# Optimization experiments

Measured on AMD Instinct MI355X. Metric: run time of the kernel, lower is better.

## Reference

```python
import jax, jax.numpy as jnp
import numpy as np

SEQ, D, H, FF = 2048, 1024, 16, 4096
HD = D // H  # head_dim = 64


def setup_inputs() -> dict:
    key = jax.random.key(0)
    ks = jax.random.split(key, 13)
    s = lambda k, shape, fan_in: jax.random.normal(k, shape, jnp.float32) / np.sqrt(fan_in)
    return {
        "x":  jax.random.normal(ks[0], (SEQ, D), jnp.float32),
        # per-head Q/K/V linears, batched over the head axis: [H, D, HD]
        "Wq": s(ks[1], (H, D, HD), D), "bq": jnp.zeros((H, HD), jnp.float32),
        "Wk": s(ks[2], (H, D, HD), D), "bk": jnp.zeros((H, HD), jnp.float32),
        "Wv": s(ks[3], (H, D, HD), D), "bv": jnp.zeros((H, HD), jnp.float32),
        "Wp": s(ks[4], (D, D), D),     "bp": jnp.zeros((D,), jnp.float32),
        "W1": s(ks[5], (D, FF), D),    "b1": jnp.zeros((FF,), jnp.float32),
        "W2": s(ks[6], (FF, D), FF),   "b2": jnp.zeros((D,), jnp.float32),
    }


def reference(x, Wq, bq, Wk, bk, Wv, bv, Wp, bp, W1, b1, W2, b2):
    # Batched per-head projections: [H, S, HD]
    Qx = jnp.einsum("sd,hde->hse", x, Wq) + bq[:, None, :]
    Kx = jnp.einsum("sd,hde->hse", x, Wk) + bk[:, None, :]
    Vx = jnp.einsum("sd,hde->hse", x, Wv) + bv[:, None, :]
    # scores[h,s,t] = Qx[h,s]. Kx[h,t] / sqrt(HD); softmax over t (last dim)
    scores = jnp.einsum("hse,hte->hst", Qx, Kx) / jnp.sqrt(jnp.float32(HD))
    attn = jax.nn.softmax(scores, axis=-1)
    # Faithful to source: head[t,e] = sum_s Vx[s,e] * attn[s,t]  (attn^T @ V)
    heads = jnp.einsum("hse,hst->hte", Vx, attn)  # [H, S, HD]
    # concat heads along feature dim (head-major order) -> [S, D]
    concat = jnp.transpose(heads, (1, 0, 2)).reshape(SEQ, H * HD)
    proj = concat @ Wp + bp
    hidden = jax.nn.relu(proj @ W1 + b1)
    out = hidden @ W2 + b2
    return out
```

## Files before the change

kernel.cpp:

```cpp
#include <hip/hip_runtime.h>
#include <math.h>

constexpr int S_  = 2048;
constexpr int D_  = 1024;
constexpr int H_  = 16;
constexpr int HD_ = 64;
constexpr int FF_ = 4096;

typedef short bf16x8 __attribute__((ext_vector_type(8)));
typedef float f32x4  __attribute__((ext_vector_type(4)));

static __device__ __forceinline__ ushort f2bf(float f) {
    union { __bf16 b; ushort u; } c;
    c.b = (__bf16)f;
    return c.u;
}
static __device__ __forceinline__ float bf2f(ushort u) {
    return __uint_as_float(((unsigned)u) << 16);
}

static __device__ __forceinline__ float exp8(float x) {
    return __builtin_amdgcn_exp2f(x * 0.18033688f);
}

static __device__ __forceinline__ void gload_lds16(const void* g, void* l) {
    __builtin_amdgcn_global_load_lds(
        (const __attribute__((address_space(1))) unsigned int*)g,
        (__attribute__((address_space(3))) unsigned int*)l, 16, 0, 0);
}

static __device__ __forceinline__ void tc_tile(
    const float* __restrict__ in, ushort* __restrict__ out,
    int K, int N, int n0, int k0)
{
    __shared__ float Ts[32][33];
    const int tid = threadIdx.x;
    const int r = tid >> 3, c4 = (tid & 7) * 4;
    float4 v = *(const float4*)(in + (size_t)(k0 + r) * N + n0 + c4);
    Ts[r][c4 + 0] = v.x; Ts[r][c4 + 1] = v.y;
    Ts[r][c4 + 2] = v.z; Ts[r][c4 + 3] = v.w;
    __syncthreads();
    ushort4 o;
    o.x = f2bf(Ts[c4 + 0][r]); o.y = f2bf(Ts[c4 + 1][r]);
    o.z = f2bf(Ts[c4 + 2][r]); o.w = f2bf(Ts[c4 + 3][r]);
    *(ushort4*)(out + (size_t)(n0 + r) * K + k0 + c4) = o;
}

__global__ __launch_bounds__(256) void pack_all(
    const float* __restrict__ x,
    const float* __restrict__ Wq, const float* __restrict__ Wk,
    const float* __restrict__ Wv, const float* __restrict__ Wp,
    const float* __restrict__ W1, const float* __restrict__ W2,
    const float* __restrict__ bq, const float* __restrict__ bk,
    const float* __restrict__ bv,
    ushort* __restrict__ xb, ushort* __restrict__ BTqkv,
    ushort* __restrict__ BTp, ushort* __restrict__ BT1,
    ushort* __restrict__ BT2, float* __restrict__ biascat)
{
    const int b = blockIdx.x;
    const int tid = threadIdx.x;
    if (b < 2048) {
        const int i = b * 1024 + tid * 4;
        float4 v = *(const float4*)(x + i);
        ushort4 o;
        o.x = f2bf(v.x); o.y = f2bf(v.y); o.z = f2bf(v.z); o.w = f2bf(v.w);
        *(ushort4*)(xb + i) = o;
    } else if (b < 5120) {
        int j = b - 2048;
        const int which = j >> 10;
        j &= 1023;
        const int hh = j >> 6, t = j & 63;
        const float* W = (which == 0) ? Wq : (which == 1) ? Wk : Wv;
        tc_tile(W + hh * 65536, BTqkv + which * 1024 * 1024 + hh * 65536,
                1024, 64, (t & 1) * 32, (t >> 1) * 32);
    } else if (b < 6144) {
        const int j = b - 5120;
        tc_tile(Wp, BTp, 1024, 1024, (j & 31) * 32, (j >> 5) * 32);
    } else if (b < 10240) {
        const int j = b - 6144;
        tc_tile(W1, BT1, 1024, 4096, (j & 127) * 32, (j >> 7) * 32);
    } else if (b < 14336) {
        const int j = b - 10240;
        tc_tile(W2, BT2, 4096, 1024, (j & 31) * 32, (j >> 5) * 32);
    } else {
        const int i = (b - 14336) * 256 + tid;
        float v = (i < 1024) ? bq[i] : (i < 2048 ? bk[i - 1024] : bv[i - 2048]);
        biascat[i] = v;
    }
}

template <int BM, int BN, int WR, int WC, int KS, int RELU, int OUT>
__global__ __launch_bounds__(WR * WC * 64) void gemm_mfma(
    const ushort* __restrict__ A, const ushort* __restrict__ BT,
    const float* __restrict__ bias, void* __restrict__ Cv,
    void* __restrict__ Cv2, int M, int N, int K)
{
    constexpr int WAVES = WR * WC;
    constexpr int WTM = BM / WR, WTN = BN / WC;
    constexpr int MT = WTM / 16, NT = WTN / 16;
    constexpr int AI = BM / 8;
    constexpr int TI = (BM + BN) / 8;
    constexpr int PW = TI / WAVES;

    __shared__ ushort As[BM * 64];
    __shared__ ushort Bs[BN * 64];

    const int tid = threadIdx.x;
    const int lane = tid & 63;
    const int wave = tid >> 6;
    const int wr = wave / WC, wc = wave % WC;
    const int row16 = lane & 15, kgrp = lane >> 4;
    const int m0 = blockIdx.y * BM, n0 = blockIdx.x * BN;
    const int kOff = (KS > 1) ? blockIdx.z * (K / KS) : 0;

    const int lrow = lane >> 3;
    const int sc8 = (lane & 7) ^ lrow;

    f32x4 acc[MT][NT];
#pragma unroll
    for (int i = 0; i < MT; ++i)
#pragma unroll
        for (int j = 0; j < NT; ++j) acc[i][j] = (f32x4){0.f, 0.f, 0.f, 0.f};

    for (int k0 = kOff; k0 < kOff + K / KS; k0 += 64) {
        __syncthreads();
#pragma unroll
        for (int i = 0; i < PW; ++i) {
            const int inst = wave * PW + i;
            if (inst < AI) {
                const int row = inst * 8;
                gload_lds16(A + (size_t)(m0 + row + lrow) * K + k0 + sc8 * 8,
                            As + row * 64);
            } else {
                const int row = (inst - AI) * 8;
                gload_lds16(BT + (size_t)(n0 + row + lrow) * K + k0 + sc8 * 8,
                            Bs + row * 64);
            }
        }
        __syncthreads();
#pragma unroll
        for (int ks = 0; ks < 2; ++ks) {
            bf16x8 af[MT], bfr[NT];
#pragma unroll
            for (int mt = 0; mt < MT; ++mt) {
                const int r = wr * WTM + mt * 16 + row16;
                af[mt] = *(const bf16x8*)(As + r * 64 + (((ks * 4 + kgrp) ^ (r & 7)) * 8));
            }
#pragma unroll
            for (int nt = 0; nt < NT; ++nt) {
                const int r = wc * WTN + nt * 16 + row16;
                bfr[nt] = *(const bf16x8*)(Bs + r * 64 + (((ks * 4 + kgrp) ^ (r & 7)) * 8));
            }
#pragma unroll
            for (int mt = 0; mt < MT; ++mt)
#pragma unroll
                for (int nt = 0; nt < NT; ++nt)
                    acc[mt][nt] = __builtin_amdgcn_mfma_f32_16x16x32_bf16(
                        af[mt], bfr[nt], acc[mt][nt], 0, 0, 0);
        }
    }

    if constexpr (OUT == 2) {
        float* Cp = ((blockIdx.z < KS / 2) ? (float*)Cv : (float*)Cv2)
                    + (size_t)(blockIdx.z % (KS / 2)) * M * N;
#pragma unroll
        for (int nt = 0; nt < NT; ++nt) {
            const int n = n0 + wc * WTN + nt * 16 + row16;
#pragma unroll
            for (int mt = 0; mt < MT; ++mt)
#pragma unroll
                for (int r = 0; r < 4; ++r) {
                    const int m = m0 + wr * WTM + mt * 16 + kgrp * 4 + r;
                    Cp[(size_t)m * N + n] = acc[mt][nt][r];
                }
        }
    } else if constexpr (OUT == 3) {
        ushort* QKo = (ushort*)Cv;
        ushort* VTo = (ushort*)Cv2;
        if (n0 < 2048) {
#pragma unroll
            for (int nt = 0; nt < NT; ++nt) {
                const int n = n0 + wc * WTN + nt * 16 + row16;
                const float bb = bias[n];
#pragma unroll
                for (int mt = 0; mt < MT; ++mt)
#pragma unroll
                    for (int r = 0; r < 4; ++r) {
                        const int m = m0 + wr * WTM + mt * 16 + kgrp * 4 + r;
                        QKo[(size_t)m * 2048 + n] = f2bf(acc[mt][nt][r] + bb);
                    }
            }
        } else {
#pragma unroll
            for (int nt = 0; nt < NT; ++nt) {
                const int n = n0 + wc * WTN + nt * 16 + row16;
                const float bb = bias[n];
#pragma unroll
                for (int mt = 0; mt < MT; ++mt) {
                    const int mb = m0 + wr * WTM + mt * 16 + kgrp * 4;
                    ushort4 o;
                    o.x = f2bf(acc[mt][nt][0] + bb);
                    o.y = f2bf(acc[mt][nt][1] + bb);
                    o.z = f2bf(acc[mt][nt][2] + bb);
                    o.w = f2bf(acc[mt][nt][3] + bb);
                    *(ushort4*)(VTo + (size_t)(n - 2048) * 2048 + mb) = o;
                }
            }
        }
    } else {
#pragma unroll
        for (int nt = 0; nt < NT; ++nt) {
            const int n = n0 + wc * WTN + nt * 16 + row16;
            const float bb = bias ? bias[n] : 0.f;
#pragma unroll
            for (int mt = 0; mt < MT; ++mt)
#pragma unroll
                for (int r = 0; r < 4; ++r) {
                    const int m = m0 + wr * WTM + mt * 16 + kgrp * 4 + r;
                    float v = acc[mt][nt][r] + bb;
                    if (RELU) v = fmaxf(v, 0.f);
                    if (OUT == 1)
                        ((ushort*)Cv)[(size_t)m * N + n] = f2bf(v);
                    else
                        ((float*)Cv)[(size_t)m * N + n] = v;
                }
        }
    }
}

__global__ __launch_bounds__(256) void reduce4_bias(
    const float* __restrict__ pA, const float* __restrict__ pB,
    const float* __restrict__ bias, float* __restrict__ out, int MN, int N)
{
    const int i = (blockIdx.x * 256 + threadIdx.x) * 4;
    float4 a = *(const float4*)(pA + i);
    const float4 b = *(const float4*)(pA + (size_t)MN + i);
    const float4 c = *(const float4*)(pB + i);
    const float4 d = *(const float4*)(pB + (size_t)MN + i);
    const float4 e = *(const float4*)(bias + (i & (N - 1)));
    a.x += b.x + c.x + d.x + e.x;
    a.y += b.y + c.y + d.y + e.y;
    a.z += b.z + c.z + d.z + e.z;
    a.w += b.w + c.w + d.w + e.w;
    *(float4*)(out + i) = a;
}

__global__ __launch_bounds__(256) void reduce2_bias_bf16(
    const float* __restrict__ pA, const float* __restrict__ pB,
    const float* __restrict__ bias, ushort* __restrict__ out, int N)
{
    const int i = (blockIdx.x * 256 + threadIdx.x) * 4;
    const float4 a = *(const float4*)(pA + i);
    const float4 b = *(const float4*)(pB + i);
    const float4 e = *(const float4*)(bias + (i & (N - 1)));
    ushort4 o;
    o.x = f2bf(a.x + b.x + e.x);
    o.y = f2bf(a.y + b.y + e.y);
    o.z = f2bf(a.z + b.z + e.z);
    o.w = f2bf(a.w + b.w + e.w);
    *(ushort4*)(out + i) = o;
}

__global__ __launch_bounds__(256) void attn_stats(
    const ushort* __restrict__ QK, float* __restrict__ part)
{
    const int h = blockIdx.y;
    const int s0 = blockIdx.x * 128;
    const int tz = blockIdx.z;
    const int tid = threadIdx.x;
    const int lane = tid & 63;
    const int w = tid >> 6;
    const int row16 = lane & 15;
    const int kgrp = lane >> 4;

    __shared__ ushort Ks[64 * 64];

    bf16x8 qf[2][2];
#pragma unroll
    for (int mt = 0; mt < 2; ++mt) {
        const ushort* qp = QK + (size_t)(s0 + w * 32 + mt * 16 + row16) * 2048 + h * 64;
        qf[mt][0] = *(const bf16x8*)(qp + kgrp * 8);
        qf[mt][1] = *(const bf16x8*)(qp + kgrp * 8 + 32);
    }

    float suml[2][4] = {{0.f}};
    const int lr = lane >> 3;
    const int sw8 = ((lane & 7) ^ lr) * 8;

    for (int ti = 0; ti < 8; ++ti) {
        const int t0 = tz * 512 + ti * 64;
        __syncthreads();
#pragma unroll
        for (int i = 0; i < 2; ++i) {
            const int inst = w * 2 + i;
            gload_lds16(QK + (size_t)(t0 + inst * 8 + lr) * 2048 + 1024 + h * 64 + sw8,
                        Ks + inst * 512);
        }
        __syncthreads();
#pragma unroll
        for (int nt = 0; nt < 4; ++nt) {
            const int kr = nt * 16 + row16;
            bf16x8 kf0 = *(const bf16x8*)(Ks + kr * 64 + ((kgrp ^ (kr & 7)) * 8));
            bf16x8 kf1 = *(const bf16x8*)(Ks + kr * 64 + (((kgrp + 4) ^ (kr & 7)) * 8));
#pragma unroll
            for (int mt = 0; mt < 2; ++mt) {
                f32x4 sc = (f32x4){0.f, 0.f, 0.f, 0.f};
                sc = __builtin_amdgcn_mfma_f32_16x16x32_bf16(qf[mt][0], kf0, sc, 0, 0, 0);
                sc = __builtin_amdgcn_mfma_f32_16x16x32_bf16(qf[mt][1], kf1, sc, 0, 0, 0);
#pragma unroll
                for (int r = 0; r < 4; ++r)
                    suml[mt][r] += exp8(sc[r]);
            }
        }
    }
#pragma unroll
    for (int mt = 0; mt < 2; ++mt)
#pragma unroll
        for (int r = 0; r < 4; ++r) {
#pragma unroll
            for (int m = 1; m < 16; m <<= 1)
                suml[mt][r] += __shfl_xor(suml[mt][r], m, 64);
        }
    if (row16 == 0) {
#pragma unroll
        for (int mt = 0; mt < 2; ++mt)
#pragma unroll
            for (int r = 0; r < 4; ++r)
                part[((size_t)tz * H_ + h) * S_ + s0 + w * 32 + mt * 16 + kgrp * 4 + r]
                    = suml[mt][r];
    }
}

__global__ __launch_bounds__(256) void vscale_fused(
    ushort* __restrict__ VT, const float* __restrict__ statsP)
{
    const int s0 = blockIdx.x * 128;
    const int h = blockIdx.y;
    const int tid = threadIdx.x;
    __shared__ float il[128];
    if (tid < 128) {
        const int HS = H_ * S_;
        const int idx = h * S_ + s0 + tid;
        float s = statsP[idx] + statsP[HS + idx] +
                  statsP[2 * HS + idx] + statsP[3 * HS + idx];
        il[tid] = 1.f / s;
    }
    __syncthreads();
#pragma unroll
    for (int c = tid; c < 1024; c += 256) {
        const int row = c >> 4, cc = (c & 15) * 8;
        const size_t off = (size_t)(h * 64 + row) * 2048 + s0 + cc;
        union { uint4 u; ushort s[8]; } v;
        v.u = *(const uint4*)(VT + off);
#pragma unroll
        for (int j = 0; j < 8; ++j)
            v.s[j] = f2bf(bf2f(v.s[j]) * il[cc + j]);
        *(uint4*)(VT + off) = v.u;
    }
}

__global__ __launch_bounds__(256) void attn_pv(
    const ushort* __restrict__ QK, const ushort* __restrict__ VT,
    ushort* __restrict__ pvp)
{
    const int h = blockIdx.y;
    const int t0 = blockIdx.x * 128;
    const int sbase = blockIdx.z * 512;
    const int tid = threadIdx.x;
    const int lane = tid & 63;
    const int w = tid >> 6;
    const int row16 = lane & 15;
    const int kgrp = lane >> 4;

    __shared__ ushort KP[128 * 64];
    __shared__ ushort Qs[64 * 64];
    __shared__ ushort Vs[64 * 64];

    const int lr = lane >> 3;
    const int sw8 = ((lane & 7) ^ lr) * 8;

#pragma unroll
    for (int i = 0; i < 4; ++i) {
        const int inst = w * 4 + i;
        gload_lds16(QK + (size_t)(t0 + inst * 8 + lr) * 2048 + 1024 + h * 64 + sw8,
                    KP + inst * 512);
    }
    __syncthreads();
    bf16x8 kf[8][2];
#pragma unroll
    for (int nt = 0; nt < 8; ++nt) {
        const int r = nt * 16 + row16;
        kf[nt][0] = *(const bf16x8*)(KP + r * 64 + ((kgrp ^ (r & 7)) * 8));
        kf[nt][1] = *(const bf16x8*)(KP + r * 64 + (((kgrp + 4) ^ (r & 7)) * 8));
    }

    f32x4 acc[2][4];
#pragma unroll
    for (int i = 0; i < 2; ++i)
#pragma unroll
        for (int j = 0; j < 4; ++j) acc[i][j] = (f32x4){0.f, 0.f, 0.f, 0.f};

    for (int si = 0; si < 8; ++si) {
        const int s0 = sbase + si * 64;
        __syncthreads();
#pragma unroll
        for (int i = 0; i < 2; ++i) {
            const int inst = w * 2 + i;
            const int r = inst * 8 + lr;
            gload_lds16(QK + (size_t)(s0 + r) * 2048 + h * 64 + sw8,
                        Qs + inst * 512);
            gload_lds16(VT + (size_t)(h * 64 + r) * 2048 + s0 + sw8,
                        Vs + inst * 512);
        }
        __syncthreads();

        const int qr = w * 16 + row16;
        bf16x8 qf0 = *(const bf16x8*)(Qs + qr * 64 + ((kgrp ^ (qr & 7)) * 8));
        bf16x8 qf1 = *(const bf16x8*)(Qs + qr * 64 + (((kgrp + 4) ^ (qr & 7)) * 8));
#pragma unroll
        for (int nt = 0; nt < 8; ++nt) {
            f32x4 sc = (f32x4){0.f, 0.f, 0.f, 0.f};
            sc = __builtin_amdgcn_mfma_f32_16x16x32_bf16(qf0, kf[nt][0], sc, 0, 0, 0);
            sc = __builtin_amdgcn_mfma_f32_16x16x32_bf16(qf1, kf[nt][1], sc, 0, 0, 0);
            ushort4 o;
            o.x = f2bf(exp8(sc[0]));
            o.y = f2bf(exp8(sc[1]));
            o.z = f2bf(exp8(sc[2]));
            o.w = f2bf(exp8(sc[3]));
            const int tl = nt * 16 + row16;
            const int chunk = w * 2 + (kgrp >> 1);
            *(ushort4*)(KP + tl * 64 + ((chunk ^ (tl & 7)) * 8) + (kgrp & 1) * 4) = o;
        }
        __syncthreads();

        bf16x8 vf[4][2];
#pragma unroll
        for (int nt = 0; nt < 4; ++nt) {
            const int vr = nt * 16 + row16;
            vf[nt][0] = *(const bf16x8*)(Vs + vr * 64 + ((kgrp ^ (vr & 7)) * 8));
            vf[nt][1] = *(const bf16x8*)(Vs + vr * 64 + (((kgrp + 4) ^ (vr & 7)) * 8));
        }
#pragma unroll
        for (int mt = 0; mt < 2; ++mt) {
            const int pr = w * 32 + mt * 16 + row16;
            bf16x8 pf0 = *(const bf16x8*)(KP + pr * 64 + ((kgrp ^ (pr & 7)) * 8));
            bf16x8 pf1 = *(const bf16x8*)(KP + pr * 64 + (((kgrp + 4) ^ (pr & 7)) * 8));
#pragma unroll
            for (int nt = 0; nt < 4; ++nt) {
                acc[mt][nt] = __builtin_amdgcn_mfma_f32_16x16x32_bf16(pf0, vf[nt][0], acc[mt][nt], 0, 0, 0);
                acc[mt][nt] = __builtin_amdgcn_mfma_f32_16x16x32_bf16(pf1, vf[nt][1], acc[mt][nt], 0, 0, 0);
            }
        }
    }

    ushort* dst = pvp + (size_t)blockIdx.z * S_ * D_;
#pragma unroll
    for (int mt = 0; mt < 2; ++mt)
#pragma unroll
        for (int nt = 0; nt < 4; ++nt)
#pragma unroll
            for (int r = 0; r < 4; ++r) {
                const int t = t0 + w * 32 + mt * 16 + kgrp * 4 + r;
                const int e = nt * 16 + row16;
                dst[(size_t)t * D_ + h * 64 + e] = f2bf(acc[mt][nt][r]);
            }
}

__global__ __launch_bounds__(256) void reduce_cat(
    const ushort* __restrict__ p, ushort* __restrict__ concat)
{
    const size_t SD = (size_t)S_ * D_;
    const size_t i = ((size_t)blockIdx.x * 256 + threadIdx.x) * 8;
    union { uint4 u; ushort s[8]; } a, b, c, d, o;
    a.u = *(const uint4*)(p + i);
    b.u = *(const uint4*)(p + SD + i);
    c.u = *(const uint4*)(p + 2 * SD + i);
    d.u = *(const uint4*)(p + 3 * SD + i);
#pragma unroll
    for (int j = 0; j < 8; ++j)
        o.s[j] = f2bf(bf2f(a.s[j]) + bf2f(b.s[j]) + bf2f(c.s[j]) + bf2f(d.s[j]));
    *(uint4*)(concat + i) = o.u;
}

extern "C" void kernel_launch(void* const* d_in, const int* in_sizes, int n_in,
                              void* d_out, int out_size, void* d_ws,
                              size_t ws_size, hipStream_t stream)
{
    const float* x  = (const float*)d_in[0];
    const float* Wq = (const float*)d_in[1];
    const float* bq = (const float*)d_in[2];
    const float* Wk = (const float*)d_in[3];
    const float* bk = (const float*)d_in[4];
    const float* Wv = (const float*)d_in[5];
    const float* bv = (const float*)d_in[6];
    const float* Wp = (const float*)d_in[7];
    const float* bp = (const float*)d_in[8];
    const float* W1 = (const float*)d_in[9];
    const float* b1 = (const float*)d_in[10];
    const float* W2 = (const float*)d_in[11];
    const float* b2 = (const float*)d_in[12];
    float* out = (float*)d_out;

    constexpr size_t MB = 1u << 20;
    char* base = (char*)d_ws;
    ushort* BT2    = (ushort*)(base +  0 * MB);
    ushort* BT1    = (ushort*)(base +  8 * MB);
    ushort* BTp    = (ushort*)(base + 16 * MB);
    ushort* xb     = (ushort*)(base + 18 * MB);
    ushort* concat = (ushort*)(base + 18 * MB);
    ushort* BTqkv  = (ushort*)(base + 22 * MB);
    ushort* projb  = (ushort*)(base + 22 * MB);
    ushort* QKcat  = (ushort*)(base + 28 * MB);
    ushort* VTg    = (ushort*)(base + 36 * MB);
    ushort* pvp    = (ushort*)(base + 40 * MB);
    float*  prjA   = (float*) (base + 28 * MB);
    float*  prjB   = (float*) (base + 36 * MB);
    ushort* hidden = (ushort*)(base + 28 * MB);
    float*  ff2a   = (float*) (base + 44 * MB);
    float*  ff2b   = (float*) (base +  8 * MB);
    float*  biascat= (float*) (base + 60 * MB);
    float*  statsP = biascat + 4096;

    pack_all<<<dim3(14348), 256, 0, stream>>>(
        x, Wq, Wk, Wv, Wp, W1, W2, bq, bk, bv,
        xb, BTqkv, BTp, BT1, BT2, biascat);

    gemm_mfma<128, 128, 2, 2, 1, 0, 3>
        <<<dim3(3072 / 128, S_ / 128, 1), 256, 0, stream>>>(
            xb, BTqkv, biascat, QKcat, VTg, S_, 3072, D_);

    attn_stats<<<dim3(S_ / 128, H_, 4), 256, 0, stream>>>(QKcat, statsP);

    vscale_fused<<<dim3(S_ / 128, H_), 256, 0, stream>>>(VTg, statsP);

    attn_pv<<<dim3(S_ / 128, H_, 4), 256, 0, stream>>>(QKcat, VTg, pvp);

    reduce_cat<<<dim3(S_ * D_ / 2048), 256, 0, stream>>>(pvp, concat);

    gemm_mfma<64, 128, 1, 4, 2, 0, 2>
        <<<dim3(D_ / 128, S_ / 64, 2), 256, 0, stream>>>(
            concat, BTp, nullptr, prjA, prjB, S_, D_, D_);
    reduce2_bias_bf16<<<dim3(S_ * D_ / 1024), 256, 0, stream>>>(
        prjA, prjB, bp, projb, D_);

    gemm_mfma<128, 128, 2, 2, 1, 1, 1>
        <<<dim3(FF_ / 128, S_ / 128, 1), 256, 0, stream>>>(
            projb, BT1, b1, hidden, nullptr, S_, FF_, D_);

    gemm_mfma<128, 128, 2, 2, 4, 0, 2>
        <<<dim3(D_ / 128, S_ / 128, 4), 256, 0, stream>>>(
            hidden, BT2, nullptr, ff2a, ff2b, S_, D_, FF_);

    reduce4_bias<<<dim3(S_ * D_ / 1024), 256, 0, stream>>>(
        ff2a, ff2b, b2, out, S_ * D_, D_);
}
```

Before: 272.7 us.

## Fuse softmax normalization into attn_pv and double-buffer K/Q/V tile loads

Removes the separate vscale_fused kernel. attn_pv now reads the partial row sums, forms 1/l in shared memory and multiplies each exp'd score by it before the PV MFMA, instead of rescaling V in global memory in a separate pass. Both attention kernels now double-buffer their K (stats) or Q/V (pv) tiles in LDS, prefetching the next tile while the current one is computed. attn_pv's wave work is also reassigned so each wave owns 32 key rows, which keeps P writes and reads wave-local and drops one barrier per iteration. The cost is more LDS per block and register changes, which could lower occupancy.

New measurement: 267.8 us. Within noise of the previous version (-1.8%).

```diff
diff --git a/kernel.cpp b/kernel.cpp
--- a/kernel.cpp
+++ b/kernel.cpp
@@ -273,7 +273,7 @@
     const int row16 = lane & 15;
     const int kgrp = lane >> 4;
 
-    __shared__ ushort Ks[64 * 64];
+    __shared__ ushort Ks[2][64 * 64];
 
     bf16x8 qf[2][2];
 #pragma unroll
@@ -287,21 +287,31 @@
     const int lr = lane >> 3;
     const int sw8 = ((lane & 7) ^ lr) * 8;
 
+#pragma unroll
+    for (int i = 0; i < 2; ++i) {
+        const int inst = w * 2 + i;
+        gload_lds16(QK + (size_t)(tz * 512 + inst * 8 + lr) * 2048 + 1024 + h * 64 + sw8,
+                    Ks[0] + inst * 512);
+    }
+
     for (int ti = 0; ti < 8; ++ti) {
-        const int t0 = tz * 512 + ti * 64;
         __syncthreads();
-#pragma unroll
-        for (int i = 0; i < 2; ++i) {
-            const int inst = w * 2 + i;
-            gload_lds16(QK + (size_t)(t0 + inst * 8 + lr) * 2048 + 1024 + h * 64 + sw8,
-                        Ks + inst * 512);
-        }
-        __syncthreads();
+        if (ti < 7) {
+            const int t1 = tz * 512 + (ti + 1) * 64;
+            ushort* kb = Ks[(ti + 1) & 1];
+#pragma unroll
+            for (int i = 0; i < 2; ++i) {
+                const int inst = w * 2 + i;
+                gload_lds16(QK + (size_t)(t1 + inst * 8 + lr) * 2048 + 1024 + h * 64 + sw8,
+                            kb + inst * 512);
+            }
+        }
+        const ushort* Kb = Ks[ti & 1];
 #pragma unroll
         for (int nt = 0; nt < 4; ++nt) {
             const int kr = nt * 16 + row16;
-            bf16x8 kf0 = *(const bf16x8*)(Ks + kr * 64 + ((kgrp ^ (kr & 7)) * 8));
-            bf16x8 kf1 = *(const bf16x8*)(Ks + kr * 64 + (((kgrp + 4) ^ (kr & 7)) * 8));
+            bf16x8 kf0 = *(const bf16x8*)(Kb + kr * 64 + ((kgrp ^ (kr & 7)) * 8));
+            bf16x8 kf1 = *(const bf16x8*)(Kb + kr * 64 + (((kgrp + 4) ^ (kr & 7)) * 8));
 #pragma unroll
             for (int mt = 0; mt < 2; ++mt) {
                 f32x4 sc = (f32x4){0.f, 0.f, 0.f, 0.f};
@@ -331,37 +341,9 @@
     }
 }
 
-__global__ __launch_bounds__(256) void vscale_fused(
-    ushort* __restrict__ VT, const float* __restrict__ statsP)
-{
-    const int s0 = blockIdx.x * 128;
-    const int h = blockIdx.y;
-    const int tid = threadIdx.x;
-    __shared__ float il[128];
-    if (tid < 128) {
-        const int HS = H_ * S_;
-        const int idx = h * S_ + s0 + tid;
-        float s = statsP[idx] + statsP[HS + idx] +
-                  statsP[2 * HS + idx] + statsP[3 * HS + idx];
-        il[tid] = 1.f / s;
-    }
-    __syncthreads();
-#pragma unroll
-    for (int c = tid; c < 1024; c += 256) {
-        const int row = c >> 4, cc = (c & 15) * 8;
-        const size_t off = (size_t)(h * 64 + row) * 2048 + s0 + cc;
-        union { uint4 u; ushort s[8]; } v;
-        v.u = *(const uint4*)(VT + off);
-#pragma unroll
-        for (int j = 0; j < 8; ++j)
-            v.s[j] = f2bf(bf2f(v.s[j]) * il[cc + j]);
-        *(uint4*)(VT + off) = v.u;
-    }
-}
-
 __global__ __launch_bounds__(256) void attn_pv(
     const ushort* __restrict__ QK, const ushort* __restrict__ VT,
-    ushort* __restrict__ pvp)
+    const float* __restrict__ statsP, ushort* __restrict__ pvp)
 {
     const int h = blockIdx.y;
     const int t0 = blockIdx.x * 128;
@@ -373,8 +355,9 @@
     const int kgrp = lane >> 4;
 
     __shared__ ushort KP[128 * 64];
-    __shared__ ushort Qs[64 * 64];
-    __shared__ ushort Vs[64 * 64];
+    __shared__ ushort Qs[2][64 * 64];
+    __shared__ ushort Vs[2][64 * 64];
+    __shared__ float  ilL[512];
 
     const int lr = lane >> 3;
     const int sw8 = ((lane & 7) ^ lr) * 8;
@@ -385,11 +368,30 @@
         gload_lds16(QK + (size_t)(t0 + inst * 8 + lr) * 2048 + 1024 + h * 64 + sw8,
                     KP + inst * 512);
     }
+#pragma unroll
+    for (int i = 0; i < 2; ++i) {
+        const int inst = w * 2 + i;
+        const int r = inst * 8 + lr;
+        gload_lds16(QK + (size_t)(sbase + r) * 2048 + h * 64 + sw8, Qs[0] + inst * 512);
+        gload_lds16(VT + (size_t)(h * 64 + r) * 2048 + sbase + sw8, Vs[0] + inst * 512);
+    }
+    {
+        const int HS = H_ * S_;
+#pragma unroll
+        for (int k = 0; k < 2; ++k) {
+            const int sl = tid * 2 + k;
+            const int idx = h * S_ + sbase + sl;
+            float s = statsP[idx] + statsP[HS + idx] +
+                      statsP[2 * HS + idx] + statsP[3 * HS + idx];
+            ilL[sl] = 1.f / s;
+        }
+    }
     __syncthreads();
-    bf16x8 kf[8][2];
-#pragma unroll
-    for (int nt = 0; nt < 8; ++nt) {
-        const int r = nt * 16 + row16;
+
+    bf16x8 kf[2][2];
+#pragma unroll
+    for (int nt = 0; nt < 2; ++nt) {
+        const int r = w * 32 + nt * 16 + row16;
         kf[nt][0] = *(const bf16x8*)(KP + r * 64 + ((kgrp ^ (r & 7)) * 8));
         kf[nt][1] = *(const bf16x8*)(KP + r * 64 + (((kgrp + 4) ^ (r & 7)) * 8));
     }
@@ -401,44 +403,50 @@
         for (int j = 0; j < 4; ++j) acc[i][j] = (f32x4){0.f, 0.f, 0.f, 0.f};
 
     for (int si = 0; si < 8; ++si) {
-        const int s0 = sbase + si * 64;
-        __syncthreads();
-#pragma unroll
-        for (int i = 0; i < 2; ++i) {
-            const int inst = w * 2 + i;
-            const int r = inst * 8 + lr;
-            gload_lds16(QK + (size_t)(s0 + r) * 2048 + h * 64 + sw8,
-                        Qs + inst * 512);
-            gload_lds16(VT + (size_t)(h * 64 + r) * 2048 + s0 + sw8,
-                        Vs + inst * 512);
-        }
-        __syncthreads();
-
-        const int qr = w * 16 + row16;
-        bf16x8 qf0 = *(const bf16x8*)(Qs + qr * 64 + ((kgrp ^ (qr & 7)) * 8));
-        bf16x8 qf1 = *(const bf16x8*)(Qs + qr * 64 + (((kgrp + 4) ^ (qr & 7)) * 8));
-#pragma unroll
-        for (int nt = 0; nt < 8; ++nt) {
-            f32x4 sc = (f32x4){0.f, 0.f, 0.f, 0.f};
-            sc = __builtin_amdgcn_mfma_f32_16x16x32_bf16(qf0, kf[nt][0], sc, 0, 0, 0);
-            sc = __builtin_amdgcn_mfma_f32_16x16x32_bf16(qf1, kf[nt][1], sc, 0, 0, 0);
-            ushort4 o;
-            o.x = f2bf(exp8(sc[0]));
-            o.y = f2bf(exp8(sc[1]));
-            o.z = f2bf(exp8(sc[2]));
-            o.w = f2bf(exp8(sc[3]));
-            const int tl = nt * 16 + row16;
-            const int chunk = w * 2 + (kgrp >> 1);
-            *(ushort4*)(KP + tl * 64 + ((chunk ^ (tl & 7)) * 8) + (kgrp & 1) * 4) = o;
-        }
-        __syncthreads();
+        if (si > 0) __syncthreads();
+        if (si < 7) {
+            const int s1 = sbase + (si + 1) * 64;
+            ushort* qb = Qs[(si + 1) & 1];
+            ushort* vb = Vs[(si + 1) & 1];
+#pragma unroll
+            for (int i = 0; i < 2; ++i) {
+                const int inst = w * 2 + i;
+                const int r = inst * 8 + lr;
+                gload_lds16(QK + (size_t)(s1 + r) * 2048 + h * 64 + sw8, qb + inst * 512);
+                gload_lds16(VT + (size_t)(h * 64 + r) * 2048 + s1 + sw8, vb + inst * 512);
+            }
+        }
+        const ushort* Qb = Qs[si & 1];
+        const ushort* Vb = Vs[si & 1];
+
+#pragma unroll
+        for (int mt = 0; mt < 4; ++mt) {
+            const int qr = mt * 16 + row16;
+            bf16x8 qf0 = *(const bf16x8*)(Qb + qr * 64 + ((kgrp ^ (qr & 7)) * 8));
+            bf16x8 qf1 = *(const bf16x8*)(Qb + qr * 64 + (((kgrp + 4) ^ (qr & 7)) * 8));
+            f32x4 il4 = *(const f32x4*)(ilL + si * 64 + mt * 16 + kgrp * 4);
+#pragma unroll
+            for (int nt = 0; nt < 2; ++nt) {
+                f32x4 sc = (f32x4){0.f, 0.f, 0.f, 0.f};
+                sc = __builtin_amdgcn_mfma_f32_16x16x32_bf16(qf0, kf[nt][0], sc, 0, 0, 0);
+                sc = __builtin_amdgcn_mfma_f32_16x16x32_bf16(qf1, kf[nt][1], sc, 0, 0, 0);
+                ushort4 o;
+                o.x = f2bf(exp8(sc[0]) * il4[0]);
+                o.y = f2bf(exp8(sc[1]) * il4[1]);
+                o.z = f2bf(exp8(sc[2]) * il4[2]);
+                o.w = f2bf(exp8(sc[3]) * il4[3]);
+                const int tl = w * 32 + nt * 16 + row16;
+                const int chunk = mt * 2 + (kgrp >> 1);
+                *(ushort4*)(KP + tl * 64 + ((chunk ^ (tl & 7)) * 8) + (kgrp & 1) * 4) = o;
+            }
+        }
 
         bf16x8 vf[4][2];
 #pragma unroll
         for (int nt = 0; nt < 4; ++nt) {
             const int vr = nt * 16 + row16;
-            vf[nt][0] = *(const bf16x8*)(Vs + vr * 64 + ((kgrp ^ (vr & 7)) * 8));
-            vf[nt][1] = *(const bf16x8*)(Vs + vr * 64 + (((kgrp + 4) ^ (vr & 7)) * 8));
+            vf[nt][0] = *(const bf16x8*)(Vb + vr * 64 + ((kgrp ^ (vr & 7)) * 8));
+            vf[nt][1] = *(const bf16x8*)(Vb + vr * 64 + (((kgrp + 4) ^ (vr & 7)) * 8));
         }
 #pragma unroll
         for (int mt = 0; mt < 2; ++mt) {
@@ -531,9 +539,7 @@
 
     attn_stats<<<dim3(S_ / 128, H_, 4), 256, 0, stream>>>(QKcat, statsP);
 
-    vscale_fused<<<dim3(S_ / 128, H_), 256, 0, stream>>>(VTg, statsP);
-
-    attn_pv<<<dim3(S_ / 128, H_, 4), 256, 0, stream>>>(QKcat, VTg, pvp);
+    attn_pv<<<dim3(S_ / 128, H_, 4), 256, 0, stream>>>(QKcat, VTg, statsP, pvp);
 
     reduce_cat<<<dim3(S_ * D_ / 2048), 256, 0, stream>>>(pvp, concat);
 
```
